# Kernel optimization log

Measured on AMD Instinct MI355X. Metric: run time of the kernel, lower is better.

## Reference

```python
import jax, jax.numpy as jnp
import numpy as np

REG_DIAG = 0.01   # per-position regularizer added inside the loop in the original
REG_EPS = 1e-05   # global regularizer added after the loop


def setup_inputs() -> dict:
    key = jax.random.key(0)
    B, C, HW = 32, 128, 3136
    embedding = jax.random.normal(key, (B, C, HW), dtype=jnp.float32)
    return {"embedding": embedding}


def reference(embedding):
    # embedding: (B, C, HW)
    B, C, HW = embedding.shape
    mean = jnp.mean(embedding, axis=0)                     # (C, HW)
    centered = embedding - mean[None, :, :]                # (B, C, HW)
    # Per-position sample covariance: cov[i] = X_m^T X_m / (B-1), X_m = (B, C) slice at position i.
    cov = jnp.einsum('bci,bdi->icd', centered, centered) / (B - 1)  # (HW, C, C)
    eye = jnp.eye(C, dtype=embedding.dtype)
    cov = cov + (REG_DIAG + REG_EPS) * eye[None, :, :]
    inv_covariance = jnp.linalg.inv(cov)                   # batched inverse, (HW, C, C)
    return (mean, inv_covariance)
```

## Files before the change

kernel.cpp:

```cpp
#include <hip/hip_runtime.h>

#define HW 3136
#define NB 32
#define NC 128
#define XST 132
#define SST 36
#define LAMV 0.01001f
#define SIG(r) (((((r) & 1)) << 4) | ((r) >> 1))

static __device__ __forceinline__ float2 pka0(float2 c, float2 v, float2 a) {
  float2 d;
  asm("v_pk_fma_f32 %0, %1, %2, %3 op_sel:[0,0,0] op_sel_hi:[0,1,1]"
      : "=v"(d) : "v"(c), "v"(v), "v"(a));
  return d;
}
static __device__ __forceinline__ float2 pka1(float2 c, float2 v, float2 a) {
  float2 d;
  asm("v_pk_fma_f32 %0, %1, %2, %3 op_sel:[1,0,0] op_sel_hi:[1,1,1]"
      : "=v"(d) : "v"(c), "v"(v), "v"(a));
  return d;
}
static __device__ __forceinline__ float2 pke(float2 a, float2 b, float2 c) {
  float2 d;
  asm("v_pk_fma_f32 %0, %1, %2, %3"
      : "=v"(d) : "v"(a), "v"(b), "v"(c));
  return d;
}

__global__ __launch_bounds__(512, 8)
void mvg_kernel(const float* __restrict__ emb, float* __restrict__ out) {
  const int bid = blockIdx.x;
  const int pos = (bid & 7) * 392 + (bid >> 3);
  const int t = threadIdx.x;

  __shared__ __align__(16) float XcB[NB * XST];
  __shared__ __align__(16) float WB[NB * XST];
  __shared__ __align__(16) float SB[32 * SST];
  __shared__ float ms[NC];

  #pragma unroll
  for (int m = 0; m < 8; ++m) {
    const int idx = t + 512 * m;
    const int b = idx >> 7;
    const int c = idx & (NC - 1);
    XcB[SIG(b) * XST + c] = emb[(size_t)b * (size_t)(NC * HW) + (size_t)c * HW + pos];
  }
  __syncthreads();

  if (t < NC) {
    float s = 0.f;
    #pragma unroll
    for (int b = 0; b < NB; ++b) s += XcB[b * XST + t];
    const float m = s * (1.0f / NB);
    ms[t] = m;
    out[(size_t)t * HW + pos] = m;
  }
  __syncthreads();

  #pragma unroll
  for (int m = 0; m < 8; ++m) {
    const int idx = t + 512 * m;
    const int b = idx >> 7;
    const int c = idx & (NC - 1);
    XcB[b * XST + c] -= ms[c];
  }
  __syncthreads();

  if (t < 256) {
    const int I = t >> 4;
    const int J = t & 15;
    const float* xi0 = &XcB[I * XST];
    const float* xi1 = &XcB[(16 + I) * XST];
    const float* xj0 = &XcB[J * XST];
    const float* xj1 = &XcB[(16 + J) * XST];
    float2 d00 = make_float2(0.f, 0.f), d01 = make_float2(0.f, 0.f);
    float2 d10 = make_float2(0.f, 0.f), d11 = make_float2(0.f, 0.f);
    #pragma unroll 8
    for (int c = 0; c < NC; c += 4) {
      const float4 a0 = *(const float4*)&xi0[c];
      const float4 a1 = *(const float4*)&xi1[c];
      const float4 b0 = *(const float4*)&xj0[c];
      const float4 b1 = *(const float4*)&xj1[c];
      const float2 a0L = make_float2(a0.x, a0.y), a0H = make_float2(a0.z, a0.w);
      const float2 a1L = make_float2(a1.x, a1.y), a1H = make_float2(a1.z, a1.w);
      const float2 b0L = make_float2(b0.x, b0.y), b0H = make_float2(b0.z, b0.w);
      const float2 b1L = make_float2(b1.x, b1.y), b1H = make_float2(b1.z, b1.w);
      d00 = pke(a0L, b0L, d00); d00 = pke(a0H, b0H, d00);
      d01 = pke(a0L, b1L, d01); d01 = pke(a0H, b1H, d01);
      d10 = pke(a1L, b0L, d10); d10 = pke(a1H, b0H, d10);
      d11 = pke(a1L, b1L, d11); d11 = pke(a1H, b1H, d11);
    }
    const float s31 = 1.0f / 31.0f;
    const float dg = (I == J) ? LAMV : 0.f;
    float2 e0, e1;
    e0.x = (d00.x + d00.y) * s31 + dg;
    e0.y = (d01.x + d01.y) * s31;
    e1.x = (d10.x + d10.y) * s31;
    e1.y = (d11.x + d11.y) * s31 + dg;
    *(float2*)&SB[I * SST + 2 * J] = e0;
    *(float2*)&SB[(16 + I) * SST + 2 * J] = e1;
  }
  __syncthreads();

  if (t < 64) {
    const int r = t & 31;
    const int hb = (t >> 5) << 4;
    const int rs = SIG(r);
    float m[16];
    #pragma unroll
    for (int j = 0; j < 4; ++j) {
      const float4 v = *(const float4*)&SB[rs * SST + hb + 4 * j];
      m[4 * j] = v.x; m[4 * j + 1] = v.y; m[4 * j + 2] = v.z; m[4 * j + 3] = v.w;
    }

    #define SWEEP_K(K) {                                                    \
      float pc = m[(K) & 15] - ((r == (K)) ? 1.0f : 0.0f);                  \
      const float dm1 = __shfl(pc, (((K) >> 4) << 5) + (K), 64);            \
      const float cr  = __shfl(pc, (((K) >> 4) << 5) + r, 64);              \
      const float g = cr * __builtin_amdgcn_rcpf(dm1 + 1.0f);               \
      float hj[16];                                                         \
      _Pragma("unroll")                                                     \
      for (int j = 0; j < 16; ++j)                                          \
        hj[j] = __shfl(pc, (((K) >> 4) << 5) + hb + j, 64);                 \
      _Pragma("unroll")                                                     \
      for (int j = 0; j < 16; ++j) m[j] = fmaf(-g, hj[j], m[j]);            \
    }

    SWEEP_K(0)  SWEEP_K(1)  SWEEP_K(2)  SWEEP_K(3)
    SWEEP_K(4)  SWEEP_K(5)  SWEEP_K(6)  SWEEP_K(7)
    SWEEP_K(8)  SWEEP_K(9)  SWEEP_K(10) SWEEP_K(11)
    SWEEP_K(12) SWEEP_K(13) SWEEP_K(14) SWEEP_K(15)
    SWEEP_K(16) SWEEP_K(17) SWEEP_K(18) SWEEP_K(19)
    SWEEP_K(20) SWEEP_K(21) SWEEP_K(22) SWEEP_K(23)
    SWEEP_K(24) SWEEP_K(25) SWEEP_K(26) SWEEP_K(27)
    SWEEP_K(28) SWEEP_K(29) SWEEP_K(30) SWEEP_K(31)

    #pragma unroll
    for (int j = 0; j < 16; ++j) {
      const int col = hb + j;
      SB[rs * SST + col] = (col == r) ? (2.0f - m[j]) : (-m[j]);
    }
  }
  __syncthreads();

  if (t < 256) {
    const int s2 = t >> 4;
    const int C0 = (t & 15) << 3;
    float2 w0[4], w1[4];
    #pragma unroll
    for (int q = 0; q < 4; ++q) {
      w0[q] = make_float2(0.f, 0.f);
      w1[q] = make_float2(0.f, 0.f);
    }
    #pragma unroll 2
    for (int j = 0; j < 32; j += 4) {
      const float4 sv0 = *(const float4*)&SB[s2 * SST + j];
      const float4 sv1 = *(const float4*)&SB[(16 + s2) * SST + j];
      const float2 s0L = make_float2(sv0.x, sv0.y), s0H = make_float2(sv0.z, sv0.w);
      const float2 s1L = make_float2(sv1.x, sv1.y), s1H = make_float2(sv1.z, sv1.w);
      const int jh = j >> 1;
      const float* xr0 = &XcB[jh * XST + C0];
      const float* xr1 = &XcB[(16 + jh) * XST + C0];
      const float* xr2 = &XcB[(jh + 1) * XST + C0];
      const float* xr3 = &XcB[(16 + jh + 1) * XST + C0];
      {
        const float4 a = *(const float4*)xr0;
        const float4 b = *(const float4*)(xr0 + 4);
        w0[0] = pka0(s0L, make_float2(a.x, a.y), w0[0]);
        w0[1] = pka0(s0L, make_float2(a.z, a.w), w0[1]);
        w0[2] = pka0(s0L, make_float2(b.x, b.y), w0[2]);
        w0[3] = pka0(s0L, make_float2(b.z, b.w), w0[3]);
        w1[0] = pka0(s1L, make_float2(a.x, a.y), w1[0]);
        w1[1] = pka0(s1L, make_float2(a.z, a.w), w1[1]);
        w1[2] = pka0(s1L, make_float2(b.x, b.y), w1[2]);
        w1[3] = pka0(s1L, make_float2(b.z, b.w), w1[3]);
      }
      {
        const float4 a = *(const float4*)xr1;
        const float4 b = *(const float4*)(xr1 + 4);
        w0[0] = pka1(s0L, make_float2(a.x, a.y), w0[0]);
        w0[1] = pka1(s0L, make_float2(a.z, a.w), w0[1]);
        w0[2] = pka1(s0L, make_float2(b.x, b.y), w0[2]);
        w0[3] = pka1(s0L, make_float2(b.z, b.w), w0[3]);
        w1[0] = pka1(s1L, make_float2(a.x, a.y), w1[0]);
        w1[1] = pka1(s1L, make_float2(a.z, a.w), w1[1]);
        w1[2] = pka1(s1L, make_float2(b.x, b.y), w1[2]);
        w1[3] = pka1(s1L, make_float2(b.z, b.w), w1[3]);
      }
      {
        const float4 a = *(const float4*)xr2;
        const float4 b = *(const float4*)(xr2 + 4);
        w0[0] = pka0(s0H, make_float2(a.x, a.y), w0[0]);
        w0[1] = pka0(s0H, make_float2(a.z, a.w), w0[1]);
        w0[2] = pka0(s0H, make_float2(b.x, b.y), w0[2]);
        w0[3] = pka0(s0H, make_float2(b.z, b.w), w0[3]);
        w1[0] = pka0(s1H, make_float2(a.x, a.y), w1[0]);
        w1[1] = pka0(s1H, make_float2(a.z, a.w), w1[1]);
        w1[2] = pka0(s1H, make_float2(b.x, b.y), w1[2]);
        w1[3] = pka0(s1H, make_float2(b.z, b.w), w1[3]);
      }
      {
        const float4 a = *(const float4*)xr3;
        const float4 b = *(const float4*)(xr3 + 4);
        w0[0] = pka1(s0H, make_float2(a.x, a.y), w0[0]);
        w0[1] = pka1(s0H, make_float2(a.z, a.w), w0[1]);
        w0[2] = pka1(s0H, make_float2(b.x, b.y), w0[2]);
        w0[3] = pka1(s0H, make_float2(b.z, b.w), w0[3]);
        w1[0] = pka1(s1H, make_float2(a.x, a.y), w1[0]);
        w1[1] = pka1(s1H, make_float2(a.z, a.w), w1[1]);
        w1[2] = pka1(s1H, make_float2(b.x, b.y), w1[2]);
        w1[3] = pka1(s1H, make_float2(b.z, b.w), w1[3]);
      }
    }
    *(float4*)&WB[s2 * XST + C0]     = make_float4(w0[0].x, w0[0].y, w0[1].x, w0[1].y);
    *(float4*)&WB[s2 * XST + C0 + 4] = make_float4(w0[2].x, w0[2].y, w0[3].x, w0[3].y);
    *(float4*)&WB[(16 + s2) * XST + C0]     = make_float4(w1[0].x, w1[0].y, w1[1].x, w1[1].y);
    *(float4*)&WB[(16 + s2) * XST + C0 + 4] = make_float4(w1[2].x, w1[2].y, w1[3].x, w1[3].y);
  }
  __syncthreads();

  if (t < 272) {
    const int L = t >> 1;
    const int half = t & 1;
    const float fs = sqrtf(1089.0f - 8.0f * (float)L);
    const int R = (int)floorf((33.0f - fs) * 0.5f);
    const int C = R + L - (R * (33 - R)) / 2;
    const int r8 = R << 3;
    const int cb = (C << 3) + (half << 2);

    float2 aP[8][2];
    #pragma unroll
    for (int r = 0; r < 8; ++r) {
      aP[r][0] = make_float2(0.f, 0.f);
      aP[r][1] = make_float2(0.f, 0.f);
    }
    #pragma unroll 4
    for (int u = 0; u < 32; ++u) {
      const float4 cv0 = *(const float4*)&XcB[u * XST + r8];
      const float4 cv1 = *(const float4*)&XcB[u * XST + r8 + 4];
      const float4 rv  = *(const float4*)&WB[u * XST + cb];
      const float2 rL = make_float2(rv.x, rv.y), rH = make_float2(rv.z, rv.w);
      const float2 c01 = make_float2(cv0.x, cv0.y), c23 = make_float2(cv0.z, cv0.w);
      const float2 c45 = make_float2(cv1.x, cv1.y), c67 = make_float2(cv1.z, cv1.w);
      aP[0][0] = pka0(c01, rL, aP[0][0]); aP[0][1] = pka0(c01, rH, aP[0][1]);
      aP[1][0] = pka1(c01, rL, aP[1][0]); aP[1][1] = pka1(c01, rH, aP[1][1]);
      aP[2][0] = pka0(c23, rL, aP[2][0]); aP[2][1] = pka0(c23, rH, aP[2][1]);
      aP[3][0] = pka1(c23, rL, aP[3][0]); aP[3][1] = pka1(c23, rH, aP[3][1]);
      aP[4][0] = pka0(c45, rL, aP[4][0]); aP[4][1] = pka0(c45, rH, aP[4][1]);
      aP[5][0] = pka1(c45, rL, aP[5][0]); aP[5][1] = pka1(c45, rH, aP[5][1]);
      aP[6][0] = pka0(c67, rL, aP[6][0]); aP[6][1] = pka0(c67, rH, aP[6][1]);
      aP[7][0] = pka1(c67, rL, aP[7][0]); aP[7][1] = pka1(c67, rH, aP[7][1]);
    }

    const float ILAM = 1.0f / LAMV;
    const float IL31 = ILAM / 31.0f;
    float* o = out + (size_t)NC * HW + (size_t)pos * (NC * NC);

    #pragma unroll
    for (int r = 0; r < 8; ++r) {
      const int gr = r8 + r;
      float4 w;
      w.x = fmaf(-IL31, aP[r][0].x, (gr == cb + 0) ? ILAM : 0.f);
      w.y = fmaf(-IL31, aP[r][0].y, (gr == cb + 1) ? ILAM : 0.f);
      w.z = fmaf(-IL31, aP[r][1].x, (gr == cb + 2) ? ILAM : 0.f);
      w.w = fmaf(-IL31, aP[r][1].y, (gr == cb + 3) ? ILAM : 0.f);
      *(float4*)&o[(size_t)gr * NC + cb] = w;
    }

    if (R != C) {
      {
        const float4 m0 = make_float4(-IL31 * aP[0][0].x, -IL31 * aP[1][0].x,
                                      -IL31 * aP[2][0].x, -IL31 * aP[3][0].x);
        const float4 m1 = make_float4(-IL31 * aP[4][0].x, -IL31 * aP[5][0].x,
                                      -IL31 * aP[6][0].x, -IL31 * aP[7][0].x);
        *(float4*)&o[(size_t)(cb + 0) * NC + r8] = m0;
        *(float4*)&o[(size_t)(cb + 0) * NC + r8 + 4] = m1;
      }
      {
        const float4 m0 = make_float4(-IL31 * aP[0][0].y, -IL31 * aP[1][0].y,
                                      -IL31 * aP[2][0].y, -IL31 * aP[3][0].y);
        const float4 m1 = make_float4(-IL31 * aP[4][0].y, -IL31 * aP[5][0].y,
                                      -IL31 * aP[6][0].y, -IL31 * aP[7][0].y);
        *(float4*)&o[(size_t)(cb + 1) * NC + r8] = m0;
        *(float4*)&o[(size_t)(cb + 1) * NC + r8 + 4] = m1;
      }
      {
        const float4 m0 = make_float4(-IL31 * aP[0][1].x, -IL31 * aP[1][1].x,
                                      -IL31 * aP[2][1].x, -IL31 * aP[3][1].x);
        const float4 m1 = make_float4(-IL31 * aP[4][1].x, -IL31 * aP[5][1].x,
                                      -IL31 * aP[6][1].x, -IL31 * aP[7][1].x);
        *(float4*)&o[(size_t)(cb + 2) * NC + r8] = m0;
        *(float4*)&o[(size_t)(cb + 2) * NC + r8 + 4] = m1;
      }
      {
        const float4 m0 = make_float4(-IL31 * aP[0][1].y, -IL31 * aP[1][1].y,
                                      -IL31 * aP[2][1].y, -IL31 * aP[3][1].y);
        const float4 m1 = make_float4(-IL31 * aP[4][1].y, -IL31 * aP[5][1].y,
                                      -IL31 * aP[6][1].y, -IL31 * aP[7][1].y);
        *(float4*)&o[(size_t)(cb + 3) * NC + r8] = m0;
        *(float4*)&o[(size_t)(cb + 3) * NC + r8 + 4] = m1;
      }
    }
  }
}

extern "C" void kernel_launch(void* const* d_in, const int* in_sizes, int n_in,
                              void* d_out, int out_size, void* d_ws, size_t ws_size,
                              hipStream_t stream) {
  const float* emb = (const float*)d_in[0];
  float* out = (float*)d_out;
  mvg_kernel<<<HW, 512, 0, stream>>>(emb, out);
}
```

Baseline: 145.8 us.

## Exploit Gram symmetry, use LDS pivot broadcast, and remap W column tiles

The 32x32 Gram product now computes only the upper-triangular 2x2 blocks (136 threads instead of 256) and mirrors them into the lower half. The Gauss-Jordan sweep broadcasts each pivot column through a shared buffer with vector LDS reads instead of 18 cross-lane shuffles per step. The W = S·X stage splits each thread's columns into two separated 4-wide chunks to change the LDS bank access pattern. The pivot buffer reuses the mean array and relies on same-wave ordering without a barrier, which adds a correctness risk if the two wavefront halves diverge.

```diff
diff --git a/kernel.cpp b/kernel.cpp
--- a/kernel.cpp
+++ b/kernel.cpp
@@ -36,7 +36,8 @@
   __shared__ __align__(16) float XcB[NB * XST];
   __shared__ __align__(16) float WB[NB * XST];
   __shared__ __align__(16) float SB[32 * SST];
-  __shared__ float ms[NC];
+  __shared__ __align__(16) float ms[NC];
+  float* pivbuf = ms;
 
   #pragma unroll
   for (int m = 0; m < 8; ++m) {
@@ -66,9 +67,10 @@
   }
   __syncthreads();
 
-  if (t < 256) {
-    const int I = t >> 4;
-    const int J = t & 15;
+  if (t < 136) {
+    const float fs = sqrtf(1089.0f - 8.0f * (float)t);
+    const int I = (int)floorf((33.0f - fs) * 0.5f);
+    const int J = I + t - (I * (33 - I)) / 2;
     const float* xi0 = &XcB[I * XST];
     const float* xi1 = &XcB[(16 + I) * XST];
     const float* xj0 = &XcB[J * XST];
@@ -99,12 +101,17 @@
     e1.y = (d11.x + d11.y) * s31 + dg;
     *(float2*)&SB[I * SST + 2 * J] = e0;
     *(float2*)&SB[(16 + I) * SST + 2 * J] = e1;
+    if (I != J) {
+      *(float2*)&SB[J * SST + 2 * I] = make_float2(e0.x, e1.x);
+      *(float2*)&SB[(16 + J) * SST + 2 * I] = make_float2(e0.y, e1.y);
+    }
   }
   __syncthreads();
 
   if (t < 64) {
     const int r = t & 31;
-    const int hb = (t >> 5) << 4;
+    const int hbit = t >> 5;
+    const int hb = hbit << 4;
     const int rs = SIG(r);
     float m[16];
     #pragma unroll
@@ -114,16 +121,25 @@
     }
 
     #define SWEEP_K(K) {                                                    \
-      float pc = m[(K) & 15] - ((r == (K)) ? 1.0f : 0.0f);                  \
-      const float dm1 = __shfl(pc, (((K) >> 4) << 5) + (K), 64);            \
-      const float cr  = __shfl(pc, (((K) >> 4) << 5) + r, 64);              \
+      const float pc = m[(K) & 15] - ((r == (K)) ? 1.0f : 0.0f);            \
+      if (hbit == ((K) >> 4)) pivbuf[r] = pc;                               \
+      asm volatile("" ::: "memory");                                        \
+      const float dm1 = pivbuf[(K)];                                        \
+      const float cr  = pivbuf[r];                                          \
+      const float4 h0 = *(const float4*)&pivbuf[hb];                        \
+      const float4 h1 = *(const float4*)&pivbuf[hb + 4];                    \
+      const float4 h2 = *(const float4*)&pivbuf[hb + 8];                    \
+      const float4 h3 = *(const float4*)&pivbuf[hb + 12];                   \
+      asm volatile("" ::: "memory");                                        \
       const float g = cr * __builtin_amdgcn_rcpf(dm1 + 1.0f);               \
-      float hj[16];                                                         \
-      _Pragma("unroll")                                                     \
-      for (int j = 0; j < 16; ++j)                                          \
-        hj[j] = __shfl(pc, (((K) >> 4) << 5) + hb + j, 64);                 \
-      _Pragma("unroll")                                                     \
-      for (int j = 0; j < 16; ++j) m[j] = fmaf(-g, hj[j], m[j]);            \
+      m[0]  = fmaf(-g, h0.x, m[0]);  m[1]  = fmaf(-g, h0.y, m[1]);          \
+      m[2]  = fmaf(-g, h0.z, m[2]);  m[3]  = fmaf(-g, h0.w, m[3]);          \
+      m[4]  = fmaf(-g, h1.x, m[4]);  m[5]  = fmaf(-g, h1.y, m[5]);          \
+      m[6]  = fmaf(-g, h1.z, m[6]);  m[7]  = fmaf(-g, h1.w, m[7]);          \
+      m[8]  = fmaf(-g, h2.x, m[8]);  m[9]  = fmaf(-g, h2.y, m[9]);          \
+      m[10] = fmaf(-g, h2.z, m[10]); m[11] = fmaf(-g, h2.w, m[11]);         \
+      m[12] = fmaf(-g, h3.x, m[12]); m[13] = fmaf(-g, h3.y, m[13]);         \
+      m[14] = fmaf(-g, h3.z, m[14]); m[15] = fmaf(-g, h3.w, m[15]);         \
     }
 
     SWEEP_K(0)  SWEEP_K(1)  SWEEP_K(2)  SWEEP_K(3)
@@ -145,7 +161,8 @@
 
   if (t < 256) {
     const int s2 = t >> 4;
-    const int C0 = (t & 15) << 3;
+    const int CA = (t & 15) << 2;
+    const int CB = 64 + CA;
     float2 w0[4], w1[4];
     #pragma unroll
     for (int q = 0; q < 4; ++q) {
@@ -159,13 +176,13 @@
       const float2 s0L = make_float2(sv0.x, sv0.y), s0H = make_float2(sv0.z, sv0.w);
       const float2 s1L = make_float2(sv1.x, sv1.y), s1H = make_float2(sv1.z, sv1.w);
       const int jh = j >> 1;
-      const float* xr0 = &XcB[jh * XST + C0];
-      const float* xr1 = &XcB[(16 + jh) * XST + C0];
-      const float* xr2 = &XcB[(jh + 1) * XST + C0];
-      const float* xr3 = &XcB[(16 + jh + 1) * XST + C0];
-      {
-        const float4 a = *(const float4*)xr0;
-        const float4 b = *(const float4*)(xr0 + 4);
+      const float* xr0 = &XcB[jh * XST];
+      const float* xr1 = &XcB[(16 + jh) * XST];
+      const float* xr2 = &XcB[(jh + 1) * XST];
+      const float* xr3 = &XcB[(17 + jh) * XST];
+      {
+        const float4 a = *(const float4*)&xr0[CA];
+        const float4 b = *(const float4*)&xr0[CB];
         w0[0] = pka0(s0L, make_float2(a.x, a.y), w0[0]);
         w0[1] = pka0(s0L, make_float2(a.z, a.w), w0[1]);
         w0[2] = pka0(s0L, make_float2(b.x, b.y), w0[2]);
@@ -176,8 +193,8 @@
         w1[3] = pka0(s1L, make_float2(b.z, b.w), w1[3]);
       }
       {
-        const float4 a = *(const float4*)xr1;
-        const float4 b = *(const float4*)(xr1 + 4);
+        const float4 a = *(const float4*)&xr1[CA];
+        const float4 b = *(const float4*)&xr1[CB];
         w0[0] = pka1(s0L, make_float2(a.x, a.y), w0[0]);
         w0[1] = pka1(s0L, make_float2(a.z, a.w), w0[1]);
         w0[2] = pka1(s0L, make_float2(b.x, b.y), w0[2]);
@@ -188,8 +205,8 @@
         w1[3] = pka1(s1L, make_float2(b.z, b.w), w1[3]);
       }
       {
-        const float4 a = *(const float4*)xr2;
-        const float4 b = *(const float4*)(xr2 + 4);
+        const float4 a = *(const float4*)&xr2[CA];
+        const float4 b = *(const float4*)&xr2[CB];
         w0[0] = pka0(s0H, make_float2(a.x, a.y), w0[0]);
         w0[1] = pka0(s0H, make_float2(a.z, a.w), w0[1]);
         w0[2] = pka0(s0H, make_float2(b.x, b.y), w0[2]);
@@ -200,8 +217,8 @@
         w1[3] = pka0(s1H, make_float2(b.z, b.w), w1[3]);
       }
       {
-        const float4 a = *(const float4*)xr3;
-        const float4 b = *(const float4*)(xr3 + 4);
+        const float4 a = *(const float4*)&xr3[CA];
+        const float4 b = *(const float4*)&xr3[CB];
         w0[0] = pka1(s0H, make_float2(a.x, a.y), w0[0]);
         w0[1] = pka1(s0H, make_float2(a.z, a.w), w0[1]);
         w0[2] = pka1(s0H, make_float2(b.x, b.y), w0[2]);
@@ -212,10 +229,10 @@
         w1[3] = pka1(s1H, make_float2(b.z, b.w), w1[3]);
       }
     }
-    *(float4*)&WB[s2 * XST + C0]     = make_float4(w0[0].x, w0[0].y, w0[1].x, w0[1].y);
-    *(float4*)&WB[s2 * XST + C0 + 4] = make_float4(w0[2].x, w0[2].y, w0[3].x, w0[3].y);
-    *(float4*)&WB[(16 + s2) * XST + C0]     = make_float4(w1[0].x, w1[0].y, w1[1].x, w1[1].y);
-    *(float4*)&WB[(16 + s2) * XST + C0 + 4] = make_float4(w1[2].x, w1[2].y, w1[3].x, w1[3].y);
+    *(float4*)&WB[s2 * XST + CA] = make_float4(w0[0].x, w0[0].y, w0[1].x, w0[1].y);
+    *(float4*)&WB[s2 * XST + CB] = make_float4(w0[2].x, w0[2].y, w0[3].x, w0[3].y);
+    *(float4*)&WB[(16 + s2) * XST + CA] = make_float4(w1[0].x, w1[0].y, w1[1].x, w1[1].y);
+    *(float4*)&WB[(16 + s2) * XST + CB] = make_float4(w1[2].x, w1[2].y, w1[3].x, w1[3].y);
   }
   __syncthreads();
 
```

New measurement: 332.0 us. 128% more time.
